# Kernel optimization log

Hardware: AMD Instinct MI355X
Metric: run time of the kernel (lower is better)

## Reference

```python
import jax, jax.numpy as jnp
import numpy as np

N_NODES = 100000
N_EDGES = 4000000
IN_DIM = 3
HID = 8
EPS = 1e-5


def _layer_norm(h, g, b):
    m = jnp.mean(h, axis=-1, keepdims=True)
    v = jnp.mean(jnp.square(h - m), axis=-1, keepdims=True)
    return (h - m) * jax.lax.rsqrt(v + EPS) * g + b


def setup_inputs() -> dict:
    key = jax.random.key(0)
    ks = jax.random.split(key, 10)
    x = jax.random.normal(ks[0], (N_NODES, IN_DIM), dtype=jnp.float32)
    edge_index = jax.random.randint(ks[1], (2, N_EDGES), 0, N_NODES, dtype=jnp.int64)

    def lin(k, fan_in, fan_out):
        bound = 1.0 / np.sqrt(fan_in)
        kw, kb = jax.random.split(k)
        W = jax.random.uniform(kw, (fan_in, fan_out), jnp.float32, -bound, bound)
        b = jax.random.uniform(kb, (fan_out,), jnp.float32, -bound, bound)
        return W, b

    W0, b0 = lin(ks[2], 2 * IN_DIM, HID)
    W1, b1 = lin(ks[3], HID, HID)
    W2, b2 = lin(ks[4], HID, HID)
    W3, b3 = lin(ks[5], HID, 1)
    g0 = jnp.ones((HID,), jnp.float32); be0 = jnp.zeros((HID,), jnp.float32)
    g1 = jnp.ones((HID,), jnp.float32); be1 = jnp.zeros((HID,), jnp.float32)
    g2 = jnp.ones((HID,), jnp.float32); be2 = jnp.zeros((HID,), jnp.float32)
    return {"x": x, "edge_index": edge_index,
            "W0": W0, "b0": b0, "g0": g0, "be0": be0,
            "W1": W1, "b1": b1, "g1": g1, "be1": be1,
            "W2": W2, "b2": b2, "g2": g2, "be2": be2,
            "W3": W3, "b3": b3}


def reference(x, edge_index, W0, b0, g0, be0, W1, b1, g1, be1, W2, b2, g2, be2, W3, b3):
    start, end = edge_index[0], edge_index[1]
    # [E, 2*IN_DIM] gathered edge inputs
    e = jnp.concatenate([x[start], x[end]], axis=1)
    h = jnp.tanh(_layer_norm(e @ W0 + b0, g0, be0))
    h = jnp.tanh(_layer_norm(h @ W1 + b1, g1, be1))
    h = jnp.tanh(_layer_norm(h @ W2 + b2, g2, be2))
    out = (h @ W3 + b3).squeeze(-1)  # [E]
    return out
```

## Files before the change

kernel.cpp:

```cpp
#include <hip/hip_runtime.h>

typedef _Float16 h2 __attribute__((ext_vector_type(2)));

#define N_EDGES 4000000
#define N_NODES 100000
#define HID 8
#define NPT 4
#define TWO_LOG2E 2.8853900817779268f
#define LN_EPS 1e-5f

#define O_GC0 0
#define O_BC0 8
#define O_GC1 16
#define O_BC1 24
#define O_GC2 32
#define O_BC2 40
#define O_B1  48
#define O_B2  56
#define O_B3  64
#define O_W1P 72
#define O_W2P 104
#define O_W3P 136
#define O_W0P 144
#define O_B0C 176
#define O_XH  256
#define WS_FLOATS_NEEDED (256 + 2 * N_NODES)

#if __has_builtin(__builtin_amdgcn_fdot2)
#define FDOT2(a, b, c) __builtin_amdgcn_fdot2((a), (b), (c), false)
#else
#define FDOT2(a, b, c) ((float)(a)[0] * (float)(b)[0] + ((float)(a)[1] * (float)(b)[1] + (c)))
#endif

__device__ void prep_hidden_layer(const float* __restrict__ W,
                                  const float* __restrict__ b,
                                  float* __restrict__ ws, uint* __restrict__ wsu,
                                  int wofs, int bofs) {
    float Wc[64];
    for (int k = 0; k < 8; ++k) {
        float rm = 0.f;
        for (int j = 0; j < 8; ++j) rm += W[k * 8 + j];
        rm *= 0.125f;
        for (int j = 0; j < 8; ++j) Wc[k * 8 + j] = -2.f * (W[k * 8 + j] - rm);
    }
    for (int k = 0; k < 8; ++k) {
        float m = 0.f;
        for (int j = 0; j < 8; ++j) m += (float)(_Float16)Wc[k * 8 + j];
        m *= 0.125f;
        for (int j = 0; j < 8; ++j) Wc[k * 8 + j] -= m;
    }
    for (int j = 0; j < 8; ++j)
        for (int q = 0; q < 4; ++q) {
            h2 v;
            v[0] = (_Float16)Wc[(2 * q) * 8 + j];
            v[1] = (_Float16)Wc[(2 * q + 1) * 8 + j];
            wsu[wofs + j * 4 + q] = __builtin_bit_cast(uint, v);
        }
    float mb = 0.f, tot = 0.f;
    for (int j = 0; j < 8; ++j) mb += b[j];
    for (int i = 0; i < 64; ++i) tot += W[i];
    for (int j = 0; j < 8; ++j) {
        float cs = 0.f;
        for (int k = 0; k < 8; ++k) cs += W[k * 8 + j];
        ws[bofs + j] = b[j] + cs - mb * 0.125f - tot * 0.125f;
    }
}

__global__ void prep_kernel(
    const float* __restrict__ x,
    const float* __restrict__ W0, const float* __restrict__ b0,
    const float* __restrict__ g0, const float* __restrict__ be0,
    const float* __restrict__ W1, const float* __restrict__ b1,
    const float* __restrict__ g1, const float* __restrict__ be1,
    const float* __restrict__ W2, const float* __restrict__ b2,
    const float* __restrict__ g2, const float* __restrict__ be2,
    const float* __restrict__ W3, const float* __restrict__ b3,
    float* __restrict__ ws, int use_tables)
{
    const int t = threadIdx.x;
    uint* wsu = reinterpret_cast<uint*>(ws);

    if (blockIdx.x == 0) {
        if (t == 0) {
            for (int j = 0; j < 8; ++j) {
                ws[O_GC0 + j] = g0[j] * TWO_LOG2E;  ws[O_BC0 + j] = be0[j] * TWO_LOG2E;
                ws[O_GC1 + j] = g1[j] * TWO_LOG2E;  ws[O_BC1 + j] = be1[j] * TWO_LOG2E;
                ws[O_GC2 + j] = g2[j] * TWO_LOG2E;  ws[O_BC2 + j] = be2[j] * TWO_LOG2E;
            }
        } else if (t == 1) {
            float Wc[48];
            for (int k = 0; k < 6; ++k) {
                float rm = 0.f;
                for (int j = 0; j < 8; ++j) rm += W0[k * 8 + j];
                rm *= 0.125f;
                for (int j = 0; j < 8; ++j) Wc[k * 8 + j] = W0[k * 8 + j] - rm;
            }
            for (int k = 0; k < 6; ++k) {
                float m = 0.f;
                for (int j = 0; j < 8; ++j) m += (float)(_Float16)Wc[k * 8 + j];
                m *= 0.125f;
                for (int j = 0; j < 8; ++j) Wc[k * 8 + j] -= m;
            }
            for (int j = 0; j < 8; ++j) {
                h2 v;
                v[0] = (_Float16)Wc[0 * 8 + j]; v[1] = (_Float16)Wc[1 * 8 + j];
                wsu[O_W0P + j * 4 + 0] = __builtin_bit_cast(uint, v);
                v[0] = (_Float16)Wc[2 * 8 + j]; v[1] = (_Float16)0.f;
                wsu[O_W0P + j * 4 + 1] = __builtin_bit_cast(uint, v);
                v[0] = (_Float16)Wc[3 * 8 + j]; v[1] = (_Float16)Wc[4 * 8 + j];
                wsu[O_W0P + j * 4 + 2] = __builtin_bit_cast(uint, v);
                v[0] = (_Float16)Wc[5 * 8 + j]; v[1] = (_Float16)0.f;
                wsu[O_W0P + j * 4 + 3] = __builtin_bit_cast(uint, v);
            }
            float bm = 0.f;
            for (int j = 0; j < 8; ++j) bm += b0[j];
            bm *= 0.125f;
            for (int j = 0; j < 8; ++j) ws[O_B0C + j] = b0[j] - bm;
        } else if (t == 2) {
            prep_hidden_layer(W1, b1, ws, wsu, O_W1P, O_B1);
        } else if (t == 3) {
            prep_hidden_layer(W2, b2, ws, wsu, O_W2P, O_B2);
        } else if (t == 4) {
            float s = 0.f;
            for (int k = 0; k < 8; ++k) s += W3[k];
            ws[O_B3] = b3[0] + s;
            for (int q = 0; q < 4; ++q) {
                h2 v;
                v[0] = (_Float16)(-2.f * W3[2 * q]);
                v[1] = (_Float16)(-2.f * W3[2 * q + 1]);
                wsu[O_W3P + q] = __builtin_bit_cast(uint, v);
            }
        }
    }

    if (use_tables) {
        const int n = blockIdx.x * blockDim.x + t;
        if (n < N_NODES) {
            const float x0 = x[n * 3 + 0], x1 = x[n * 3 + 1], x2 = x[n * 3 + 2];
            uint2 v;
            v.x = __builtin_bit_cast(uint, __builtin_amdgcn_cvt_pkrtz(x0, x1));
            v.y = __builtin_bit_cast(uint, __builtin_amdgcn_cvt_pkrtz(x2, 0.f));
            reinterpret_cast<uint2*>(ws + O_XH)[n] = v;
        }
    }
}

template<int N>
__device__ __forceinline__ void ln_pack(const float (&z)[N][HID],
                                        const float* __restrict__ gc,
                                        const float* __restrict__ bc,
                                        h2 (&p)[N][4]) {
    float r[N];
#pragma unroll
    for (int e = 0; e < N; ++e) {
        float va = 0.f;
#pragma unroll
        for (int j = 0; j < HID; ++j) va = __builtin_fmaf(z[e][j], z[e][j], va);
        r[e] = __builtin_amdgcn_rsqf(__builtin_fmaf(va, 0.125f, LN_EPS));
    }
    float e1[N][HID];
#pragma unroll
    for (int j = 0; j < HID; ++j) {
        const float gcj = gc[j], bcj = bc[j];
#pragma unroll
        for (int e = 0; e < N; ++e) {
            const float y = __builtin_fmaf(z[e][j], r[e] * gcj, bcj);
            e1[e][j] = __builtin_amdgcn_exp2f(y) + 1.0f;
        }
    }
#pragma unroll
    for (int q = 0; q < 4; ++q)
#pragma unroll
        for (int e = 0; e < N; ++e) {
            const float a = e1[e][2 * q], b = e1[e][2 * q + 1];
            const float pr = __builtin_amdgcn_rcpf(a * b);
            p[e][q] = __builtin_bit_cast(h2,
                __builtin_amdgcn_cvt_pkrtz(b * pr, a * pr));
        }
}

template<int N>
__device__ __forceinline__ void lin8_dot(const h2 (&p)[N][4],
                                         const uint* __restrict__ wp,
                                         const float* __restrict__ b,
                                         float (&zo)[N][HID]) {
#pragma unroll
    for (int j = 0; j < HID; ++j) {
        const float bj = b[j];
        const h2 w0 = __builtin_bit_cast(h2, wp[j * 4 + 0]);
        const h2 w1 = __builtin_bit_cast(h2, wp[j * 4 + 1]);
        const h2 w2 = __builtin_bit_cast(h2, wp[j * 4 + 2]);
        const h2 w3 = __builtin_bit_cast(h2, wp[j * 4 + 3]);
#pragma unroll
        for (int e = 0; e < N; ++e) {
            float acc = FDOT2(p[e][0], w0, bj);
            acc = FDOT2(p[e][1], w1, acc);
            acc = FDOT2(p[e][2], w2, acc);
            zo[e][j] = FDOT2(p[e][3], w3, acc);
        }
    }
}

template<bool UT>
__global__ __launch_bounds__(256) void edge_mlp_kernel(
    const float* __restrict__ x,
    const int*   __restrict__ ei,
    const float* __restrict__ ws,
    float* __restrict__ out)
{
    const int t = blockIdx.x * blockDim.x + threadIdx.x;
    const int base = t * NPT;
    if (base >= N_EDGES) return;

    const uint* wsu = reinterpret_cast<const uint*>(ws);
    const int4 sv = *reinterpret_cast<const int4*>(ei + base);
    const int4 dv = *reinterpret_cast<const int4*>(ei + N_EDGES + base);
    const uint si[NPT] = {(uint)sv.x, (uint)sv.y, (uint)sv.z, (uint)sv.w};
    const uint di[NPT] = {(uint)dv.x, (uint)dv.y, (uint)dv.z, (uint)dv.w};

    h2 s01[NPT], s2z[NPT], d01[NPT], d2z[NPT];
#pragma unroll
    for (int e = 0; e < NPT; ++e) {
        if (UT) {
            const uint2* XH = reinterpret_cast<const uint2*>(ws + O_XH);
            const uint2 a = XH[si[e]];
            const uint2 b = XH[di[e]];
            s01[e] = __builtin_bit_cast(h2, a.x);
            s2z[e] = __builtin_bit_cast(h2, a.y);
            d01[e] = __builtin_bit_cast(h2, b.x);
            d2z[e] = __builtin_bit_cast(h2, b.y);
        } else {
            const float s0 = x[si[e] * 3u], s1 = x[si[e] * 3u + 1], s2 = x[si[e] * 3u + 2];
            const float d0 = x[di[e] * 3u], d1 = x[di[e] * 3u + 1], d2 = x[di[e] * 3u + 2];
            s01[e] = __builtin_bit_cast(h2, __builtin_amdgcn_cvt_pkrtz(s0, s1));
            s2z[e] = __builtin_bit_cast(h2, __builtin_amdgcn_cvt_pkrtz(s2, 0.f));
            d01[e] = __builtin_bit_cast(h2, __builtin_amdgcn_cvt_pkrtz(d0, d1));
            d2z[e] = __builtin_bit_cast(h2, __builtin_amdgcn_cvt_pkrtz(d2, 0.f));
        }
    }

    float z[NPT][HID];
#pragma unroll
    for (int j = 0; j < HID; ++j) {
        const h2 wj0 = __builtin_bit_cast(h2, wsu[O_W0P + j * 4 + 0]);
        const h2 wj1 = __builtin_bit_cast(h2, wsu[O_W0P + j * 4 + 1]);
        const h2 wj2 = __builtin_bit_cast(h2, wsu[O_W0P + j * 4 + 2]);
        const h2 wj3 = __builtin_bit_cast(h2, wsu[O_W0P + j * 4 + 3]);
        const float bb = ws[O_B0C + j];
#pragma unroll
        for (int e = 0; e < NPT; ++e) {
            float a = FDOT2(s01[e], wj0, bb);
            a = FDOT2(s2z[e], wj1, a);
            a = FDOT2(d01[e], wj2, a);
            z[e][j] = FDOT2(d2z[e], wj3, a);
        }
    }

    h2 p[NPT][4];
    ln_pack<NPT>(z, ws + O_GC0, ws + O_BC0, p);
    lin8_dot<NPT>(p, wsu + O_W1P, ws + O_B1, z);
    ln_pack<NPT>(z, ws + O_GC1, ws + O_BC1, p);
    lin8_dot<NPT>(p, wsu + O_W2P, ws + O_B2, z);
    ln_pack<NPT>(z, ws + O_GC2, ws + O_BC2, p);

    const h2 w30 = __builtin_bit_cast(h2, wsu[O_W3P + 0]);
    const h2 w31 = __builtin_bit_cast(h2, wsu[O_W3P + 1]);
    const h2 w32 = __builtin_bit_cast(h2, wsu[O_W3P + 2]);
    const h2 w33 = __builtin_bit_cast(h2, wsu[O_W3P + 3]);
    const float bb3 = ws[O_B3];
    float o[NPT];
#pragma unroll
    for (int e = 0; e < NPT; ++e) {
        float acc = FDOT2(p[e][0], w30, bb3);
        acc = FDOT2(p[e][1], w31, acc);
        acc = FDOT2(p[e][2], w32, acc);
        o[e] = FDOT2(p[e][3], w33, acc);
    }

    *reinterpret_cast<float4*>(out + base) = make_float4(o[0], o[1], o[2], o[3]);
}

extern "C" void kernel_launch(void* const* d_in, const int* in_sizes, int n_in,
                              void* d_out, int out_size, void* d_ws, size_t ws_size,
                              hipStream_t stream) {
    const float* x   = (const float*)d_in[0];
    const int*   ei  = (const int*)d_in[1];
    const float* W0  = (const float*)d_in[2];
    const float* b0  = (const float*)d_in[3];
    const float* g0  = (const float*)d_in[4];
    const float* be0 = (const float*)d_in[5];
    const float* W1  = (const float*)d_in[6];
    const float* b1  = (const float*)d_in[7];
    const float* g1  = (const float*)d_in[8];
    const float* be1 = (const float*)d_in[9];
    const float* W2  = (const float*)d_in[10];
    const float* b2  = (const float*)d_in[11];
    const float* g2  = (const float*)d_in[12];
    const float* be2 = (const float*)d_in[13];
    const float* W3  = (const float*)d_in[14];
    const float* b3  = (const float*)d_in[15];
    float* out = (float*)d_out;
    float* ws  = (float*)d_ws;

    const bool ut = ws_size >= (size_t)WS_FLOATS_NEEDED * sizeof(float);
    const int prep_blocks = ut ? (N_NODES + 255) / 256 : 1;
    prep_kernel<<<prep_blocks, 256, 0, stream>>>(
        x, W0, b0, g0, be0, W1, b1, g1, be1, W2, b2, g2, be2, W3, b3,
        ws, ut ? 1 : 0);

    const int nthreads = N_EDGES / NPT;
    const int blocks = (nthreads + 255) / 256;
    if (ut)
        edge_mlp_kernel<true><<<blocks, 256, 0, stream>>>(x, ei, ws, out);
    else
        edge_mlp_kernel<false><<<blocks, 256, 0, stream>>>(x, ei, ws, out);
}
```

Baseline: 60.10 us.

## Use persistent grid with software-pipelined index loads and gathers across iterations

Replaces the one-shot grid of ~3900 blocks with a fixed 1024-block grid where each thread processes four 4-edge chunks. Index loads and node-feature gathers for later chunks are issued before the MLP compute of earlier chunks, to hide gather latency behind ALU work. This raises register pressure, which may lower occupancy, and with fewer blocks per CU there is less latency hiding from wave switching.

```diff
diff --git a/kernel.cpp b/kernel.cpp
--- a/kernel.cpp
+++ b/kernel.cpp
@@ -6,6 +6,9 @@
 #define N_NODES 100000
 #define HID 8
 #define NPT 4
+#define NBLOCKS 1024
+#define NTHREADS (NBLOCKS * 256)
+#define NITER 4
 #define TWO_LOG2E 2.8853900817779268f
 #define LN_EPS 1e-5f
 
@@ -201,6 +204,74 @@
     }
 }
 
+__device__ __forceinline__ void compute_store(
+    const h2 (&s01)[NPT], const h2 (&s2z)[NPT],
+    const h2 (&d01)[NPT], const h2 (&d2z)[NPT],
+    const float* __restrict__ ws, const uint* __restrict__ wsu,
+    float* __restrict__ out, uint b)
+{
+    float z[NPT][HID];
+#pragma unroll
+    for (int j = 0; j < HID; ++j) {
+        const h2 wj0 = __builtin_bit_cast(h2, wsu[O_W0P + j * 4 + 0]);
+        const h2 wj1 = __builtin_bit_cast(h2, wsu[O_W0P + j * 4 + 1]);
+        const h2 wj2 = __builtin_bit_cast(h2, wsu[O_W0P + j * 4 + 2]);
+        const h2 wj3 = __builtin_bit_cast(h2, wsu[O_W0P + j * 4 + 3]);
+        const float bb = ws[O_B0C + j];
+#pragma unroll
+        for (int e = 0; e < NPT; ++e) {
+            float a = FDOT2(s01[e], wj0, bb);
+            a = FDOT2(s2z[e], wj1, a);
+            a = FDOT2(d01[e], wj2, a);
+            z[e][j] = FDOT2(d2z[e], wj3, a);
+        }
+    }
+
+    h2 p[NPT][4];
+    ln_pack<NPT>(z, ws + O_GC0, ws + O_BC0, p);
+    lin8_dot<NPT>(p, wsu + O_W1P, ws + O_B1, z);
+    ln_pack<NPT>(z, ws + O_GC1, ws + O_BC1, p);
+    lin8_dot<NPT>(p, wsu + O_W2P, ws + O_B2, z);
+    ln_pack<NPT>(z, ws + O_GC2, ws + O_BC2, p);
+
+    const h2 w30 = __builtin_bit_cast(h2, wsu[O_W3P + 0]);
+    const h2 w31 = __builtin_bit_cast(h2, wsu[O_W3P + 1]);
+    const h2 w32 = __builtin_bit_cast(h2, wsu[O_W3P + 2]);
+    const h2 w33 = __builtin_bit_cast(h2, wsu[O_W3P + 3]);
+    const float bb3 = ws[O_B3];
+    float o[NPT];
+#pragma unroll
+    for (int e = 0; e < NPT; ++e) {
+        float acc = FDOT2(p[e][0], w30, bb3);
+        acc = FDOT2(p[e][1], w31, acc);
+        acc = FDOT2(p[e][2], w32, acc);
+        o[e] = FDOT2(p[e][3], w33, acc);
+    }
+    if (b < N_EDGES)
+        *reinterpret_cast<float4*>(out + b) = make_float4(o[0], o[1], o[2], o[3]);
+}
+
+__device__ __forceinline__ void gath(uint2 (&gs)[NPT], uint2 (&gd)[NPT],
+                                     const int4& s, const int4& d,
+                                     const uint2* __restrict__ XH) {
+    gs[0] = XH[(uint)s.x]; gs[1] = XH[(uint)s.y];
+    gs[2] = XH[(uint)s.z]; gs[3] = XH[(uint)s.w];
+    gd[0] = XH[(uint)d.x]; gd[1] = XH[(uint)d.y];
+    gd[2] = XH[(uint)d.z]; gd[3] = XH[(uint)d.w];
+}
+
+__device__ __forceinline__ void unpack(const uint2 (&gs)[NPT], const uint2 (&gd)[NPT],
+                                       h2 (&s01)[NPT], h2 (&s2z)[NPT],
+                                       h2 (&d01)[NPT], h2 (&d2z)[NPT]) {
+#pragma unroll
+    for (int e = 0; e < NPT; ++e) {
+        s01[e] = __builtin_bit_cast(h2, gs[e].x);
+        s2z[e] = __builtin_bit_cast(h2, gs[e].y);
+        d01[e] = __builtin_bit_cast(h2, gd[e].x);
+        d2z[e] = __builtin_bit_cast(h2, gd[e].y);
+    }
+}
+
 template<bool UT>
 __global__ __launch_bounds__(256) void edge_mlp_kernel(
     const float* __restrict__ x,
@@ -208,76 +279,70 @@
     const float* __restrict__ ws,
     float* __restrict__ out)
 {
-    const int t = blockIdx.x * blockDim.x + threadIdx.x;
-    const int base = t * NPT;
-    if (base >= N_EDGES) return;
-
+    const uint tid = blockIdx.x * 256u + threadIdx.x;
     const uint* wsu = reinterpret_cast<const uint*>(ws);
-    const int4 sv = *reinterpret_cast<const int4*>(ei + base);
-    const int4 dv = *reinterpret_cast<const int4*>(ei + N_EDGES + base);
-    const uint si[NPT] = {(uint)sv.x, (uint)sv.y, (uint)sv.z, (uint)sv.w};
-    const uint di[NPT] = {(uint)dv.x, (uint)dv.y, (uint)dv.z, (uint)dv.w};
+
+    if (!UT) {
+        for (int it = 0; it < NITER; ++it) {
+            const uint b = ((uint)it * NTHREADS + tid) * 4u;
+            if (b >= N_EDGES) return;
+            const int4 sv = *reinterpret_cast<const int4*>(ei + b);
+            const int4 dv = *reinterpret_cast<const int4*>(ei + N_EDGES + b);
+            const uint si[NPT] = {(uint)sv.x, (uint)sv.y, (uint)sv.z, (uint)sv.w};
+            const uint di[NPT] = {(uint)dv.x, (uint)dv.y, (uint)dv.z, (uint)dv.w};
+            h2 s01[NPT], s2z[NPT], d01[NPT], d2z[NPT];
+#pragma unroll
+            for (int e = 0; e < NPT; ++e) {
+                const float s0 = x[si[e] * 3u], s1 = x[si[e] * 3u + 1], s2 = x[si[e] * 3u + 2];
+                const float d0 = x[di[e] * 3u], d1 = x[di[e] * 3u + 1], d2 = x[di[e] * 3u + 2];
+                s01[e] = __builtin_bit_cast(h2, __builtin_amdgcn_cvt_pkrtz(s0, s1));
+                s2z[e] = __builtin_bit_cast(h2, __builtin_amdgcn_cvt_pkrtz(s2, 0.f));
+                d01[e] = __builtin_bit_cast(h2, __builtin_amdgcn_cvt_pkrtz(d0, d1));
+                d2z[e] = __builtin_bit_cast(h2, __builtin_amdgcn_cvt_pkrtz(d2, 0.f));
+            }
+            compute_store(s01, s2z, d01, d2z, ws, wsu, out, b);
+        }
+        return;
+    }
+
+    const uint2* XH = reinterpret_cast<const uint2*>(ws + O_XH);
+
+    const uint b0 = tid * 4u;
+    const uint b1 = (1u * NTHREADS + tid) * 4u;
+    const uint b2 = (2u * NTHREADS + tid) * 4u;
+    const uint b3 = (3u * NTHREADS + tid) * 4u;
+    const uint b3c = b3 < N_EDGES ? b3 : (N_EDGES - 4u);
+
+    int4 s0 = *reinterpret_cast<const int4*>(ei + b0);
+    int4 d0 = *reinterpret_cast<const int4*>(ei + N_EDGES + b0);
+    int4 s1 = *reinterpret_cast<const int4*>(ei + b1);
+    int4 d1 = *reinterpret_cast<const int4*>(ei + N_EDGES + b1);
+    uint2 gs0[NPT], gd0[NPT];
+    gath(gs0, gd0, s0, d0, XH);
+    int4 s2 = *reinterpret_cast<const int4*>(ei + b2);
+    int4 d2 = *reinterpret_cast<const int4*>(ei + N_EDGES + b2);
+    uint2 gs1[NPT], gd1[NPT];
+    gath(gs1, gd1, s1, d1, XH);
+    int4 s3 = *reinterpret_cast<const int4*>(ei + b3c);
+    int4 d3 = *reinterpret_cast<const int4*>(ei + N_EDGES + b3c);
 
     h2 s01[NPT], s2z[NPT], d01[NPT], d2z[NPT];
-#pragma unroll
-    for (int e = 0; e < NPT; ++e) {
-        if (UT) {
-            const uint2* XH = reinterpret_cast<const uint2*>(ws + O_XH);
-            const uint2 a = XH[si[e]];
-            const uint2 b = XH[di[e]];
-            s01[e] = __builtin_bit_cast(h2, a.x);
-            s2z[e] = __builtin_bit_cast(h2, a.y);
-            d01[e] = __builtin_bit_cast(h2, b.x);
-            d2z[e] = __builtin_bit_cast(h2, b.y);
-        } else {
-            const float s0 = x[si[e] * 3u], s1 = x[si[e] * 3u + 1], s2 = x[si[e] * 3u + 2];
-            const float d0 = x[di[e] * 3u], d1 = x[di[e] * 3u + 1], d2 = x[di[e] * 3u + 2];
-            s01[e] = __builtin_bit_cast(h2, __builtin_amdgcn_cvt_pkrtz(s0, s1));
-            s2z[e] = __builtin_bit_cast(h2, __builtin_amdgcn_cvt_pkrtz(s2, 0.f));
-            d01[e] = __builtin_bit_cast(h2, __builtin_amdgcn_cvt_pkrtz(d0, d1));
-            d2z[e] = __builtin_bit_cast(h2, __builtin_amdgcn_cvt_pkrtz(d2, 0.f));
-        }
-    }
-
-    float z[NPT][HID];
-#pragma unroll
-    for (int j = 0; j < HID; ++j) {
-        const h2 wj0 = __builtin_bit_cast(h2, wsu[O_W0P + j * 4 + 0]);
-        const h2 wj1 = __builtin_bit_cast(h2, wsu[O_W0P + j * 4 + 1]);
-        const h2 wj2 = __builtin_bit_cast(h2, wsu[O_W0P + j * 4 + 2]);
-        const h2 wj3 = __builtin_bit_cast(h2, wsu[O_W0P + j * 4 + 3]);
-        const float bb = ws[O_B0C + j];
-#pragma unroll
-        for (int e = 0; e < NPT; ++e) {
-            float a = FDOT2(s01[e], wj0, bb);
-            a = FDOT2(s2z[e], wj1, a);
-            a = FDOT2(d01[e], wj2, a);
-            z[e][j] = FDOT2(d2z[e], wj3, a);
-        }
-    }
-
-    h2 p[NPT][4];
-    ln_pack<NPT>(z, ws + O_GC0, ws + O_BC0, p);
-    lin8_dot<NPT>(p, wsu + O_W1P, ws + O_B1, z);
-    ln_pack<NPT>(z, ws + O_GC1, ws + O_BC1, p);
-    lin8_dot<NPT>(p, wsu + O_W2P, ws + O_B2, z);
-    ln_pack<NPT>(z, ws + O_GC2, ws + O_BC2, p);
-
-    const h2 w30 = __builtin_bit_cast(h2, wsu[O_W3P + 0]);
-    const h2 w31 = __builtin_bit_cast(h2, wsu[O_W3P + 1]);
-    const h2 w32 = __builtin_bit_cast(h2, wsu[O_W3P + 2]);
-    const h2 w33 = __builtin_bit_cast(h2, wsu[O_W3P + 3]);
-    const float bb3 = ws[O_B3];
-    float o[NPT];
-#pragma unroll
-    for (int e = 0; e < NPT; ++e) {
-        float acc = FDOT2(p[e][0], w30, bb3);
-        acc = FDOT2(p[e][1], w31, acc);
-        acc = FDOT2(p[e][2], w32, acc);
-        o[e] = FDOT2(p[e][3], w33, acc);
-    }
-
-    *reinterpret_cast<float4*>(out + base) = make_float4(o[0], o[1], o[2], o[3]);
+
+    uint2 gs2[NPT], gd2[NPT];
+    gath(gs2, gd2, s2, d2, XH);
+    unpack(gs0, gd0, s01, s2z, d01, d2z);
+    compute_store(s01, s2z, d01, d2z, ws, wsu, out, b0);
+
+    uint2 gs3[NPT], gd3[NPT];
+    gath(gs3, gd3, s3, d3, XH);
+    unpack(gs1, gd1, s01, s2z, d01, d2z);
+    compute_store(s01, s2z, d01, d2z, ws, wsu, out, b1);
+
+    unpack(gs2, gd2, s01, s2z, d01, d2z);
+    compute_store(s01, s2z, d01, d2z, ws, wsu, out, b2);
+
+    unpack(gs3, gd3, s01, s2z, d01, d2z);
+    compute_store(s01, s2z, d01, d2z, ws, wsu, out, b3);
 }
 
 extern "C" void kernel_launch(void* const* d_in, const int* in_sizes, int n_in,
@@ -308,10 +373,8 @@
         x, W0, b0, g0, be0, W1, b1, g1, be1, W2, b2, g2, be2, W3, b3,
         ws, ut ? 1 : 0);
 
-    const int nthreads = N_EDGES / NPT;
-    const int blocks = (nthreads + 255) / 256;
     if (ut)
-        edge_mlp_kernel<true><<<blocks, 256, 0, stream>>>(x, ei, ws, out);
+        edge_mlp_kernel<true><<<NBLOCKS, 256, 0, stream>>>(x, ei, ws, out);
     else
-        edge_mlp_kernel<false><<<blocks, 256, 0, stream>>>(x, ei, ws, out);
-}
+        edge_mlp_kernel<false><<<NBLOCKS, 256, 0, stream>>>(x, ei, ws, out);
+}
```

Measured after the change: 77.80 us. 29.5% more time.

## Gather raw node features with vector loads and drop the fp16 node table

Applied to the files above, without the earlier changes.

The prep kernel no longer builds a packed fp16 copy of the node features, so it shrinks to a single block that only prepares the weights. The edge kernel now gathers each endpoint's three floats straight from x with one 16-byte unaligned vector load and converts them to fp16 in registers. The per-thread MLP is also split into two passes of two edges each, which is meant to lower live register pressure. The intended savings are the node-table pass and its extra memory traffic. The cost is wider unaligned gathers, and the load for the last node reads one float past the end of x.

```diff
diff --git a/kernel.cpp b/kernel.cpp
--- a/kernel.cpp
+++ b/kernel.cpp
@@ -1,9 +1,10 @@
 #include <hip/hip_runtime.h>
 
 typedef _Float16 h2 __attribute__((ext_vector_type(2)));
+typedef float f4v __attribute__((ext_vector_type(4)));
+typedef f4v f4u __attribute__((aligned(4)));
 
 #define N_EDGES 4000000
-#define N_NODES 100000
 #define HID 8
 #define NPT 4
 #define TWO_LOG2E 2.8853900817779268f
@@ -23,8 +24,6 @@
 #define O_W3P 136
 #define O_W0P 144
 #define O_B0C 176
-#define O_XH  256
-#define WS_FLOATS_NEEDED (256 + 2 * N_NODES)
 
 #if __has_builtin(__builtin_amdgcn_fdot2)
 #define FDOT2(a, b, c) __builtin_amdgcn_fdot2((a), (b), (c), false)
@@ -67,7 +66,6 @@
 }
 
 __global__ void prep_kernel(
-    const float* __restrict__ x,
     const float* __restrict__ W0, const float* __restrict__ b0,
     const float* __restrict__ g0, const float* __restrict__ be0,
     const float* __restrict__ W1, const float* __restrict__ b1,
@@ -75,72 +73,59 @@
     const float* __restrict__ W2, const float* __restrict__ b2,
     const float* __restrict__ g2, const float* __restrict__ be2,
     const float* __restrict__ W3, const float* __restrict__ b3,
-    float* __restrict__ ws, int use_tables)
+    float* __restrict__ ws)
 {
     const int t = threadIdx.x;
     uint* wsu = reinterpret_cast<uint*>(ws);
 
-    if (blockIdx.x == 0) {
-        if (t == 0) {
-            for (int j = 0; j < 8; ++j) {
-                ws[O_GC0 + j] = g0[j] * TWO_LOG2E;  ws[O_BC0 + j] = be0[j] * TWO_LOG2E;
-                ws[O_GC1 + j] = g1[j] * TWO_LOG2E;  ws[O_BC1 + j] = be1[j] * TWO_LOG2E;
-                ws[O_GC2 + j] = g2[j] * TWO_LOG2E;  ws[O_BC2 + j] = be2[j] * TWO_LOG2E;
-            }
-        } else if (t == 1) {
-            float Wc[48];
-            for (int k = 0; k < 6; ++k) {
-                float rm = 0.f;
-                for (int j = 0; j < 8; ++j) rm += W0[k * 8 + j];
-                rm *= 0.125f;
-                for (int j = 0; j < 8; ++j) Wc[k * 8 + j] = W0[k * 8 + j] - rm;
-            }
-            for (int k = 0; k < 6; ++k) {
-                float m = 0.f;
-                for (int j = 0; j < 8; ++j) m += (float)(_Float16)Wc[k * 8 + j];
-                m *= 0.125f;
-                for (int j = 0; j < 8; ++j) Wc[k * 8 + j] -= m;
-            }
-            for (int j = 0; j < 8; ++j) {
-                h2 v;
-                v[0] = (_Float16)Wc[0 * 8 + j]; v[1] = (_Float16)Wc[1 * 8 + j];
-                wsu[O_W0P + j * 4 + 0] = __builtin_bit_cast(uint, v);
-                v[0] = (_Float16)Wc[2 * 8 + j]; v[1] = (_Float16)0.f;
-                wsu[O_W0P + j * 4 + 1] = __builtin_bit_cast(uint, v);
-                v[0] = (_Float16)Wc[3 * 8 + j]; v[1] = (_Float16)Wc[4 * 8 + j];
-                wsu[O_W0P + j * 4 + 2] = __builtin_bit_cast(uint, v);
-                v[0] = (_Float16)Wc[5 * 8 + j]; v[1] = (_Float16)0.f;
-                wsu[O_W0P + j * 4 + 3] = __builtin_bit_cast(uint, v);
-            }
-            float bm = 0.f;
-            for (int j = 0; j < 8; ++j) bm += b0[j];
-            bm *= 0.125f;
-            for (int j = 0; j < 8; ++j) ws[O_B0C + j] = b0[j] - bm;
-        } else if (t == 2) {
-            prep_hidden_layer(W1, b1, ws, wsu, O_W1P, O_B1);
-        } else if (t == 3) {
-            prep_hidden_layer(W2, b2, ws, wsu, O_W2P, O_B2);
-        } else if (t == 4) {
-            float s = 0.f;
-            for (int k = 0; k < 8; ++k) s += W3[k];
-            ws[O_B3] = b3[0] + s;
-            for (int q = 0; q < 4; ++q) {
-                h2 v;
-                v[0] = (_Float16)(-2.f * W3[2 * q]);
-                v[1] = (_Float16)(-2.f * W3[2 * q + 1]);
-                wsu[O_W3P + q] = __builtin_bit_cast(uint, v);
-            }
-        }
-    }
-
-    if (use_tables) {
-        const int n = blockIdx.x * blockDim.x + t;
-        if (n < N_NODES) {
-            const float x0 = x[n * 3 + 0], x1 = x[n * 3 + 1], x2 = x[n * 3 + 2];
-            uint2 v;
-            v.x = __builtin_bit_cast(uint, __builtin_amdgcn_cvt_pkrtz(x0, x1));
-            v.y = __builtin_bit_cast(uint, __builtin_amdgcn_cvt_pkrtz(x2, 0.f));
-            reinterpret_cast<uint2*>(ws + O_XH)[n] = v;
+    if (t == 0) {
+        for (int j = 0; j < 8; ++j) {
+            ws[O_GC0 + j] = g0[j] * TWO_LOG2E;  ws[O_BC0 + j] = be0[j] * TWO_LOG2E;
+            ws[O_GC1 + j] = g1[j] * TWO_LOG2E;  ws[O_BC1 + j] = be1[j] * TWO_LOG2E;
+            ws[O_GC2 + j] = g2[j] * TWO_LOG2E;  ws[O_BC2 + j] = be2[j] * TWO_LOG2E;
+        }
+    } else if (t == 1) {
+        float Wc[48];
+        for (int k = 0; k < 6; ++k) {
+            float rm = 0.f;
+            for (int j = 0; j < 8; ++j) rm += W0[k * 8 + j];
+            rm *= 0.125f;
+            for (int j = 0; j < 8; ++j) Wc[k * 8 + j] = W0[k * 8 + j] - rm;
+        }
+        for (int k = 0; k < 6; ++k) {
+            float m = 0.f;
+            for (int j = 0; j < 8; ++j) m += (float)(_Float16)Wc[k * 8 + j];
+            m *= 0.125f;
+            for (int j = 0; j < 8; ++j) Wc[k * 8 + j] -= m;
+        }
+        for (int j = 0; j < 8; ++j) {
+            h2 v;
+            v[0] = (_Float16)Wc[0 * 8 + j]; v[1] = (_Float16)Wc[1 * 8 + j];
+            wsu[O_W0P + j * 4 + 0] = __builtin_bit_cast(uint, v);
+            v[0] = (_Float16)Wc[2 * 8 + j]; v[1] = (_Float16)0.f;
+            wsu[O_W0P + j * 4 + 1] = __builtin_bit_cast(uint, v);
+            v[0] = (_Float16)Wc[3 * 8 + j]; v[1] = (_Float16)Wc[4 * 8 + j];
+            wsu[O_W0P + j * 4 + 2] = __builtin_bit_cast(uint, v);
+            v[0] = (_Float16)Wc[5 * 8 + j]; v[1] = (_Float16)0.f;
+            wsu[O_W0P + j * 4 + 3] = __builtin_bit_cast(uint, v);
+        }
+        float bm = 0.f;
+        for (int j = 0; j < 8; ++j) bm += b0[j];
+        bm *= 0.125f;
+        for (int j = 0; j < 8; ++j) ws[O_B0C + j] = b0[j] - bm;
+    } else if (t == 2) {
+        prep_hidden_layer(W1, b1, ws, wsu, O_W1P, O_B1);
+    } else if (t == 3) {
+        prep_hidden_layer(W2, b2, ws, wsu, O_W2P, O_B2);
+    } else if (t == 4) {
+        float s = 0.f;
+        for (int k = 0; k < 8; ++k) s += W3[k];
+        ws[O_B3] = b3[0] + s;
+        for (int q = 0; q < 4; ++q) {
+            h2 v;
+            v[0] = (_Float16)(-2.f * W3[2 * q]);
+            v[1] = (_Float16)(-2.f * W3[2 * q + 1]);
+            wsu[O_W3P + q] = __builtin_bit_cast(uint, v);
         }
     }
 }
@@ -201,7 +186,65 @@
     }
 }
 
-template<bool UT>
+__device__ __forceinline__ void mlp2(const f4u& vsa, const f4u& vsb,
+                                     const f4u& vda, const f4u& vdb,
+                                     const float* __restrict__ ws,
+                                     const uint* __restrict__ wsu,
+                                     float& oa, float& ob)
+{
+    h2 s01[2], s2z[2], d01[2], d2z[2];
+    s01[0] = __builtin_bit_cast(h2, __builtin_amdgcn_cvt_pkrtz(vsa[0], vsa[1]));
+    s2z[0] = __builtin_bit_cast(h2, __builtin_amdgcn_cvt_pkrtz(vsa[2], 0.f));
+    d01[0] = __builtin_bit_cast(h2, __builtin_amdgcn_cvt_pkrtz(vda[0], vda[1]));
+    d2z[0] = __builtin_bit_cast(h2, __builtin_amdgcn_cvt_pkrtz(vda[2], 0.f));
+    s01[1] = __builtin_bit_cast(h2, __builtin_amdgcn_cvt_pkrtz(vsb[0], vsb[1]));
+    s2z[1] = __builtin_bit_cast(h2, __builtin_amdgcn_cvt_pkrtz(vsb[2], 0.f));
+    d01[1] = __builtin_bit_cast(h2, __builtin_amdgcn_cvt_pkrtz(vdb[0], vdb[1]));
+    d2z[1] = __builtin_bit_cast(h2, __builtin_amdgcn_cvt_pkrtz(vdb[2], 0.f));
+
+    float z[2][HID];
+#pragma unroll
+    for (int j = 0; j < HID; ++j) {
+        const h2 wj0 = __builtin_bit_cast(h2, wsu[O_W0P + j * 4 + 0]);
+        const h2 wj1 = __builtin_bit_cast(h2, wsu[O_W0P + j * 4 + 1]);
+        const h2 wj2 = __builtin_bit_cast(h2, wsu[O_W0P + j * 4 + 2]);
+        const h2 wj3 = __builtin_bit_cast(h2, wsu[O_W0P + j * 4 + 3]);
+        const float bb = ws[O_B0C + j];
+#pragma unroll
+        for (int e = 0; e < 2; ++e) {
+            float a = FDOT2(s01[e], wj0, bb);
+            a = FDOT2(s2z[e], wj1, a);
+            a = FDOT2(d01[e], wj2, a);
+            z[e][j] = FDOT2(d2z[e], wj3, a);
+        }
+    }
+
+    h2 p[2][4];
+    ln_pack<2>(z, ws + O_GC0, ws + O_BC0, p);
+    lin8_dot<2>(p, wsu + O_W1P, ws + O_B1, z);
+    ln_pack<2>(z, ws + O_GC1, ws + O_BC1, p);
+    lin8_dot<2>(p, wsu + O_W2P, ws + O_B2, z);
+    ln_pack<2>(z, ws + O_GC2, ws + O_BC2, p);
+
+    const h2 w30 = __builtin_bit_cast(h2, wsu[O_W3P + 0]);
+    const h2 w31 = __builtin_bit_cast(h2, wsu[O_W3P + 1]);
+    const h2 w32 = __builtin_bit_cast(h2, wsu[O_W3P + 2]);
+    const h2 w33 = __builtin_bit_cast(h2, wsu[O_W3P + 3]);
+    const float bb3 = ws[O_B3];
+    {
+        float acc = FDOT2(p[0][0], w30, bb3);
+        acc = FDOT2(p[0][1], w31, acc);
+        acc = FDOT2(p[0][2], w32, acc);
+        oa = FDOT2(p[0][3], w33, acc);
+    }
+    {
+        float acc = FDOT2(p[1][0], w30, bb3);
+        acc = FDOT2(p[1][1], w31, acc);
+        acc = FDOT2(p[1][2], w32, acc);
+        ob = FDOT2(p[1][3], w33, acc);
+    }
+}
+
 __global__ __launch_bounds__(256) void edge_mlp_kernel(
     const float* __restrict__ x,
     const int*   __restrict__ ei,
@@ -215,69 +258,21 @@
     const uint* wsu = reinterpret_cast<const uint*>(ws);
     const int4 sv = *reinterpret_cast<const int4*>(ei + base);
     const int4 dv = *reinterpret_cast<const int4*>(ei + N_EDGES + base);
-    const uint si[NPT] = {(uint)sv.x, (uint)sv.y, (uint)sv.z, (uint)sv.w};
-    const uint di[NPT] = {(uint)dv.x, (uint)dv.y, (uint)dv.z, (uint)dv.w};
-
-    h2 s01[NPT], s2z[NPT], d01[NPT], d2z[NPT];
-#pragma unroll
-    for (int e = 0; e < NPT; ++e) {
-        if (UT) {
-            const uint2* XH = reinterpret_cast<const uint2*>(ws + O_XH);
-            const uint2 a = XH[si[e]];
-            const uint2 b = XH[di[e]];
-            s01[e] = __builtin_bit_cast(h2, a.x);
-            s2z[e] = __builtin_bit_cast(h2, a.y);
-            d01[e] = __builtin_bit_cast(h2, b.x);
-            d2z[e] = __builtin_bit_cast(h2, b.y);
-        } else {
-            const float s0 = x[si[e] * 3u], s1 = x[si[e] * 3u + 1], s2 = x[si[e] * 3u + 2];
-            const float d0 = x[di[e] * 3u], d1 = x[di[e] * 3u + 1], d2 = x[di[e] * 3u + 2];
-            s01[e] = __builtin_bit_cast(h2, __builtin_amdgcn_cvt_pkrtz(s0, s1));
-            s2z[e] = __builtin_bit_cast(h2, __builtin_amdgcn_cvt_pkrtz(s2, 0.f));
-            d01[e] = __builtin_bit_cast(h2, __builtin_amdgcn_cvt_pkrtz(d0, d1));
-            d2z[e] = __builtin_bit_cast(h2, __builtin_amdgcn_cvt_pkrtz(d2, 0.f));
-        }
-    }
-
-    float z[NPT][HID];
-#pragma unroll
-    for (int j = 0; j < HID; ++j) {
-        const h2 wj0 = __builtin_bit_cast(h2, wsu[O_W0P + j * 4 + 0]);
-        const h2 wj1 = __builtin_bit_cast(h2, wsu[O_W0P + j * 4 + 1]);
-        const h2 wj2 = __builtin_bit_cast(h2, wsu[O_W0P + j * 4 + 2]);
-        const h2 wj3 = __builtin_bit_cast(h2, wsu[O_W0P + j * 4 + 3]);
-        const float bb = ws[O_B0C + j];
-#pragma unroll
-        for (int e = 0; e < NPT; ++e) {
-            float a = FDOT2(s01[e], wj0, bb);
-            a = FDOT2(s2z[e], wj1, a);
-            a = FDOT2(d01[e], wj2, a);
-            z[e][j] = FDOT2(d2z[e], wj3, a);
-        }
-    }
-
-    h2 p[NPT][4];
-    ln_pack<NPT>(z, ws + O_GC0, ws + O_BC0, p);
-    lin8_dot<NPT>(p, wsu + O_W1P, ws + O_B1, z);
-    ln_pack<NPT>(z, ws + O_GC1, ws + O_BC1, p);
-    lin8_dot<NPT>(p, wsu + O_W2P, ws + O_B2, z);
-    ln_pack<NPT>(z, ws + O_GC2, ws + O_BC2, p);
-
-    const h2 w30 = __builtin_bit_cast(h2, wsu[O_W3P + 0]);
-    const h2 w31 = __builtin_bit_cast(h2, wsu[O_W3P + 1]);
-    const h2 w32 = __builtin_bit_cast(h2, wsu[O_W3P + 2]);
-    const h2 w33 = __builtin_bit_cast(h2, wsu[O_W3P + 3]);
-    const float bb3 = ws[O_B3];
-    float o[NPT];
-#pragma unroll
-    for (int e = 0; e < NPT; ++e) {
-        float acc = FDOT2(p[e][0], w30, bb3);
-        acc = FDOT2(p[e][1], w31, acc);
-        acc = FDOT2(p[e][2], w32, acc);
-        o[e] = FDOT2(p[e][3], w33, acc);
-    }
-
-    *reinterpret_cast<float4*>(out + base) = make_float4(o[0], o[1], o[2], o[3]);
+
+    const f4u vs0 = *reinterpret_cast<const f4u*>(x + (uint)sv.x * 3u);
+    const f4u vs1 = *reinterpret_cast<const f4u*>(x + (uint)sv.y * 3u);
+    const f4u vs2 = *reinterpret_cast<const f4u*>(x + (uint)sv.z * 3u);
+    const f4u vs3 = *reinterpret_cast<const f4u*>(x + (uint)sv.w * 3u);
+    const f4u vd0 = *reinterpret_cast<const f4u*>(x + (uint)dv.x * 3u);
+    const f4u vd1 = *reinterpret_cast<const f4u*>(x + (uint)dv.y * 3u);
+    const f4u vd2 = *reinterpret_cast<const f4u*>(x + (uint)dv.z * 3u);
+    const f4u vd3 = *reinterpret_cast<const f4u*>(x + (uint)dv.w * 3u);
+
+    float o0, o1, o2, o3;
+    mlp2(vs0, vs1, vd0, vd1, ws, wsu, o0, o1);
+    mlp2(vs2, vs3, vd2, vd3, ws, wsu, o2, o3);
+
+    *reinterpret_cast<float4*>(out + base) = make_float4(o0, o1, o2, o3);
 }
 
 extern "C" void kernel_launch(void* const* d_in, const int* in_sizes, int n_in,
@@ -302,16 +297,10 @@
     float* out = (float*)d_out;
     float* ws  = (float*)d_ws;
 
-    const bool ut = ws_size >= (size_t)WS_FLOATS_NEEDED * sizeof(float);
-    const int prep_blocks = ut ? (N_NODES + 255) / 256 : 1;
-    prep_kernel<<<prep_blocks, 256, 0, stream>>>(
-        x, W0, b0, g0, be0, W1, b1, g1, be1, W2, b2, g2, be2, W3, b3,
-        ws, ut ? 1 : 0);
+    prep_kernel<<<1, 64, 0, stream>>>(W0, b0, g0, be0, W1, b1, g1, be1,
+                                      W2, b2, g2, be2, W3, b3, ws);
 
     const int nthreads = N_EDGES / NPT;
     const int blocks = (nthreads + 255) / 256;
-    if (ut)
-        edge_mlp_kernel<true><<<blocks, 256, 0, stream>>>(x, ei, ws, out);
-    else
-        edge_mlp_kernel<false><<<blocks, 256, 0, stream>>>(x, ei, ws, out);
-}
+    edge_mlp_kernel<<<blocks, 256, 0, stream>>>(x, ei, ws, out);
+}
```

Result: slower. 62.64 us (+4.2%).
